# Performance work log

Measured on AMD Instinct MI355X. Metric: run time of the kernel, lower is better.

Reference implementation:

```python
import jax, jax.numpy as jnp
import numpy as np


def setup_inputs() -> dict:
    key = jax.random.key(0)
    k1, k2, k3 = jax.random.split(key, 3)
    B, D, C = 16384, 1024, 14
    z_image = jax.random.normal(k1, (B, D), dtype=jnp.float32)
    z_text = jax.random.normal(k2, (B, D), dtype=jnp.float32)
    labels = jax.random.randint(k3, (B, C), 0, 2, dtype=jnp.int32)
    return {"z_image": z_image, "z_text": z_text, "labels": labels}


def _margins(labels):
    # labels: [B, C] binary; imposter index j = (i+1) % B -> roll by -1
    lj = jnp.roll(labels, -1, axis=0)
    equal = jnp.all(labels == lj, axis=1)                     # [B]
    n = jnp.sum(labels | lj, axis=1).astype(jnp.float32)      # union size
    d = jnp.sum(labels ^ lj, axis=1).astype(jnp.float32)      # hamming diff
    m = jnp.where(n > 0, jnp.maximum(0.5, d / jnp.maximum(n, 1.0)), 0.5)
    return jnp.where(equal, 0.0, m)                           # [B]


def reference(z_image, z_text, labels):
    # similarity_function == 'dot' (default path of the torch module)
    margin = _margins(labels)                                  # [B]
    paired = jnp.sum(z_image * z_text, axis=1)                 # dot(img_i, txt_i)
    imp_img = jnp.sum(jnp.roll(z_image, -1, axis=0) * z_text, axis=1)  # dot(img_j, txt_i)
    imp_txt = jnp.sum(jnp.roll(z_text, -1, axis=0) * z_image, axis=1)  # dot(txt_j, img_i)
    loss_img = jnp.mean(jax.nn.relu(imp_img - paired + margin))
    loss_txt = jnp.mean(jax.nn.relu(imp_txt - paired + margin))
    return loss_img + loss_txt
```

## Files before the change

### kernel.cpp

```cpp
#include <hip/hip_runtime.h>


constexpr int D   = 1024;
constexpr int C   = 14;
constexpr int RPB = 8;
constexpr int CPR = D / 4;

typedef float f4 __attribute__((ext_vector_type(4)));

__device__ __forceinline__ float dot4(const f4 x, const f4 y) {
    return x.x * y.x + x.y * y.y + x.z * y.z + x.w * y.w;
}

__device__ __forceinline__ f4 shfl_down4(const f4 v) {
    f4 r;
    r.x = __shfl_down(v.x, 8, 64);
    r.y = __shfl_down(v.y, 8, 64);
    r.z = __shfl_down(v.z, 8, 64);
    r.w = __shfl_down(v.w, 8, 64);
    return r;
}

__global__ __launch_bounds__(256) void rank_phase1(
    const float* __restrict__ zi, const float* __restrict__ zt,
    const int* __restrict__ labels, float* __restrict__ partial, int B)
{
    const int wave = threadIdx.x >> 6;
    const int lane = threadIdx.x & 63;
    const int r0   = blockIdx.x * RPB;
    const int M    = B - 1;

    const int row_off = lane >> 3;
    const int cl      = lane & 7;
    const int row     = r0 + row_off;
    const int hrow    = (r0 + RPB) & M;

    const f4* ZI = (const f4*)zi;
    const f4* ZT = (const f4*)zt;

    const int cb = wave * (CPR / 4);

    float p = 0.f, ii = 0.f, it = 0.f;

    #pragma unroll
    for (int i = 0; i < CPR / 4 / 8; ++i) {
        const int c = cb + 8 * i + cl;
        const f4 a = __builtin_nontemporal_load(&ZI[(size_t)row * CPR + c]);
        const f4 b = __builtin_nontemporal_load(&ZT[(size_t)row * CPR + c]);

        f4 ha, hb;
        if (row_off == 7) {
            ha = ZI[(size_t)hrow * CPR + c];
            hb = ZT[(size_t)hrow * CPR + c];
        }

        f4 aN = shfl_down4(a);
        f4 bN = shfl_down4(b);
        if (row_off == 7) { aN = ha; bN = hb; }

        p  += dot4(a,  b);
        ii += dot4(aN, b);
        it += dot4(bN, a);
    }

    #pragma unroll
    for (int off = 1; off < 8; off <<= 1) {
        p  += __shfl_xor(p,  off, 64);
        ii += __shfl_xor(ii, off, 64);
        it += __shfl_xor(it, off, 64);
    }

    __shared__ float sm[4][RPB][3];
    if (cl == 0) {
        sm[wave][row_off][0] = p;
        sm[wave][row_off][1] = ii;
        sm[wave][row_off][2] = it;
    }
    __syncthreads();

    if (threadIdx.x < RPB) {
        const int k = threadIdx.x;
        float ps = 0.f, is = 0.f, ts = 0.f;
        #pragma unroll
        for (int w = 0; w < 4; ++w) {
            ps += sm[w][k][0];
            is += sm[w][k][1];
            ts += sm[w][k][2];
        }
        const int ra = r0 + k;
        const int rb = (ra + 1) & M;
        const int2* La = (const int2*)(labels + (size_t)ra * C);
        const int2* Lb = (const int2*)(labels + (size_t)rb * C);
        int dv = 0, nv = 0;
        #pragma unroll
        for (int q = 0; q < C / 2; ++q) {
            const int2 x = La[q];
            const int2 y = Lb[q];
            dv += (x.x ^ y.x) + (x.y ^ y.y);
            nv += (x.x | y.x) + (x.y | y.y);
        }
        const float m = (dv == 0) ? 0.f
                                  : fmaxf(0.5f, (float)dv / (float)nv);
        float v = fmaxf(is - ps + m, 0.f) + fmaxf(ts - ps + m, 0.f);
        #pragma unroll
        for (int off = 1; off < RPB; off <<= 1)
            v += __shfl_xor(v, off, 64);
        if (k == 0) partial[blockIdx.x] = v;
    }
}

__global__ __launch_bounds__(256) void rank_phase2(
    const float* __restrict__ partial, float* __restrict__ out,
    int npart, float invB)
{
    float s = 0.f;
    for (int i = threadIdx.x; i < npart; i += 256) s += partial[i];
    #pragma unroll
    for (int off = 32; off > 0; off >>= 1) s += __shfl_down(s, off, 64);
    __shared__ float sm[4];
    if ((threadIdx.x & 63) == 0) sm[threadIdx.x >> 6] = s;
    __syncthreads();
    if (threadIdx.x == 0)
        out[0] = (sm[0] + sm[1] + sm[2] + sm[3]) * invB;
}

extern "C" void kernel_launch(void* const* d_in, const int* in_sizes, int n_in,
                              void* d_out, int out_size, void* d_ws, size_t ws_size,
                              hipStream_t stream) {
    const float* zi     = (const float*)d_in[0];
    const float* zt     = (const float*)d_in[1];
    const int*   labels = (const int*)d_in[2];
    float*       out    = (float*)d_out;
    float*       ws     = (float*)d_ws;

    const int B      = in_sizes[0] / D;
    const int blocks = B / RPB;

    rank_phase1<<<blocks, 256, 0, stream>>>(zi, zt, labels, ws, B);
    rank_phase2<<<1, 256, 0, stream>>>(ws, out, blocks, 1.0f / (float)B);
}
```

Measured before the change: 155.3 us.

## Process 16 rows per block, hoist label margins before loads, drop nontemporal hints

Each block now handles 16 rows as two groups of 8, with two waves splitting the columns of each row instead of four. The label-based margin computation moves ahead of the main loop so its latency overlaps the streaming loads rather than trailing the barrier. Nontemporal loads are replaced with ordinary loads, which may let the halo row reads by neighbouring blocks hit in cache. Fewer blocks and partials are produced, at the cost of more loop iterations per wave.

```diff
diff --git a/kernel.cpp b/kernel.cpp
--- a/kernel.cpp
+++ b/kernel.cpp
@@ -3,7 +3,7 @@
 
 constexpr int D   = 1024;
 constexpr int C   = 14;
-constexpr int RPB = 8;
+constexpr int RPB = 16;
 constexpr int CPR = D / 4;
 
 typedef float f4 __attribute__((ext_vector_type(4)));
@@ -25,28 +25,48 @@
     const float* __restrict__ zi, const float* __restrict__ zt,
     const int* __restrict__ labels, float* __restrict__ partial, int B)
 {
-    const int wave = threadIdx.x >> 6;
-    const int lane = threadIdx.x & 63;
+    const int t    = threadIdx.x;
+    const int wave = t >> 6;
+    const int lane = t & 63;
     const int r0   = blockIdx.x * RPB;
     const int M    = B - 1;
 
+    const int g  = wave >> 1;
+    const int h  = wave & 1;
+
     const int row_off = lane >> 3;
     const int cl      = lane & 7;
-    const int row     = r0 + row_off;
-    const int hrow    = (r0 + RPB) & M;
+    const int row     = r0 + 8 * g + row_off;
+    const int hrow    = (r0 + 8 * g + 8) & M;
+
+    float margin = 0.f;
+    if (t < RPB) {
+        const int ra = r0 + t;
+        const int rb = (ra + 1) & M;
+        const int2* La = (const int2*)(labels + (size_t)ra * C);
+        const int2* Lb = (const int2*)(labels + (size_t)rb * C);
+        int dv = 0, nv = 0;
+        #pragma unroll
+        for (int q = 0; q < C / 2; ++q) {
+            const int2 x = La[q];
+            const int2 y = Lb[q];
+            dv += (x.x ^ y.x) + (x.y ^ y.y);
+            nv += (x.x | y.x) + (x.y | y.y);
+        }
+        margin = (dv == 0) ? 0.f : fmaxf(0.5f, (float)dv / (float)nv);
+    }
 
     const f4* ZI = (const f4*)zi;
     const f4* ZT = (const f4*)zt;
-
-    const int cb = wave * (CPR / 4);
+    const int cb = h * (CPR / 2);
 
     float p = 0.f, ii = 0.f, it = 0.f;
 
     #pragma unroll
-    for (int i = 0; i < CPR / 4 / 8; ++i) {
+    for (int i = 0; i < CPR / 2 / 8; ++i) {
         const int c = cb + 8 * i + cl;
-        const f4 a = __builtin_nontemporal_load(&ZI[(size_t)row * CPR + c]);
-        const f4 b = __builtin_nontemporal_load(&ZT[(size_t)row * CPR + c]);
+        const f4 a = ZI[(size_t)row * CPR + c];
+        const f4 b = ZT[(size_t)row * CPR + c];
 
         f4 ha, hb;
         if (row_off == 7) {
@@ -70,7 +90,7 @@
         it += __shfl_xor(it, off, 64);
     }
 
-    __shared__ float sm[4][RPB][3];
+    __shared__ float sm[4][8][3];
     if (cl == 0) {
         sm[wave][row_off][0] = p;
         sm[wave][row_off][1] = ii;
@@ -78,34 +98,18 @@
     }
     __syncthreads();
 
-    if (threadIdx.x < RPB) {
-        const int k = threadIdx.x;
-        float ps = 0.f, is = 0.f, ts = 0.f;
-        #pragma unroll
-        for (int w = 0; w < 4; ++w) {
-            ps += sm[w][k][0];
-            is += sm[w][k][1];
-            ts += sm[w][k][2];
-        }
-        const int ra = r0 + k;
-        const int rb = (ra + 1) & M;
-        const int2* La = (const int2*)(labels + (size_t)ra * C);
-        const int2* Lb = (const int2*)(labels + (size_t)rb * C);
-        int dv = 0, nv = 0;
-        #pragma unroll
-        for (int q = 0; q < C / 2; ++q) {
-            const int2 x = La[q];
-            const int2 y = Lb[q];
-            dv += (x.x ^ y.x) + (x.y ^ y.y);
-            nv += (x.x | y.x) + (x.y | y.y);
-        }
-        const float m = (dv == 0) ? 0.f
-                                  : fmaxf(0.5f, (float)dv / (float)nv);
-        float v = fmaxf(is - ps + m, 0.f) + fmaxf(ts - ps + m, 0.f);
+    if (t < RPB) {
+        const int gg = t >> 3;
+        const int lr = t & 7;
+        const float ps = sm[2 * gg][lr][0] + sm[2 * gg + 1][lr][0];
+        const float is = sm[2 * gg][lr][1] + sm[2 * gg + 1][lr][1];
+        const float ts = sm[2 * gg][lr][2] + sm[2 * gg + 1][lr][2];
+        float v = fmaxf(is - ps + margin, 0.f)
+                + fmaxf(ts - ps + margin, 0.f);
         #pragma unroll
         for (int off = 1; off < RPB; off <<= 1)
             v += __shfl_xor(v, off, 64);
-        if (k == 0) partial[blockIdx.x] = v;
+        if (t == 0) partial[blockIdx.x] = v;
     }
 }
 
```

After: 165.5 us. +6.5%, slower.
